# Performance work log

Hardware: AMD Instinct MI355X
Metric: run time of the kernel (lower is better)

The kernel has to match this reference:

```python
import jax, jax.numpy as jnp
import numpy as np
import math

B, T, DIM = 4, 4096, 1024
HID = int(DIM * 1.5)  # 1536
K = 4                  # conv kernel size
S = 16                 # num_slots
D = 384                # slot_dim


def setup_inputs() -> dict:
    key = jax.random.key(0)
    ks = jax.random.split(key, 16)
    inp = {
        "x": jax.random.normal(ks[0], (B, T, DIM), jnp.float32),
        "input_w": jax.random.normal(ks[1], (2 * HID, DIM), jnp.float32) * DIM ** -0.5,
        "conv_w": jax.random.normal(ks[2], (HID, K), jnp.float32) * K ** -0.5,
        "conv_b": jnp.zeros((HID,), jnp.float32),
        "gates_w": jax.random.normal(ks[3], (2 * HID, HID), jnp.float32) * HID ** -0.5,
        "gates_b": jnp.zeros((2 * HID,), jnp.float32),
        "forget_base": jnp.linspace(-4.323, -9.0, HID).astype(jnp.float32),
        "output_w": jax.random.normal(ks[4], (DIM, HID), jnp.float32) * HID ** -0.5,
        "memory_slots": jax.random.normal(ks[5], (S, D), jnp.float32) * 0.02,
        "wq_w": jax.random.normal(ks[6], (D, D), jnp.float32) * 0.02,
        "wk_w": jax.random.normal(ks[7], (D, HID), jnp.float32) * 0.02,
        "wv_w": jax.random.normal(ks[8], (D, HID), jnp.float32) * 0.02,
        "wg_w": jax.random.normal(ks[9], (1, HID), jnp.float32) * 0.02,
        "rq_w": jax.random.normal(ks[10], (D, HID), jnp.float32) * 0.02,
        "rk_w": jax.random.normal(ks[11], (D, D), jnp.float32) * 0.02,
        "rv_w": jax.random.normal(ks[12], (HID, D), jnp.float32) * 0.02,
    }
    return inp


def _causal_dwconv(x, w, b):
    # x: [B,T,H], w: [H,K], b: [H]; torch Conv1d(padding=K-1) then [:, :T] == causal
    xp = jnp.pad(x, ((0, 0), (K - 1, 0), (0, 0)))
    taps = jnp.stack([xp[:, j:j + T, :] for j in range(K)], axis=-1)  # [B,T,H,K]
    return jnp.einsum('bthk,hk->bth', taps, w) + b


def _scan(alpha, x):
    # h_t = alpha_t * h_{t-1} + x_t, elementwise over channels; along axis 1 (time)
    def combine(c1, c2):
        a1, b1 = c1
        a2, b2 = c2
        return a1 * a2, a2 * b1 + b2
    return jax.lax.associative_scan(combine, (alpha, x), axis=1)[1]


def reference(x, input_w, conv_w, conv_b, gates_w, gates_b, forget_base, output_w,
              memory_slots, wq_w, wk_w, wv_w, wg_w, rq_w, rk_w, rv_w):
    L = T // S  # segment length
    proj = x @ input_w.T                       # [B,T,2H]
    gate, xh = proj[..., :HID], proj[..., HID:]
    xh = _causal_dwconv(xh, conv_w, conv_b)    # [B,T,H]
    g = xh @ gates_w.T + gates_b               # [B,T,2H]
    forget, inp = g[..., :HID], g[..., HID:]
    alpha = jnp.exp(-8.0 * jax.nn.softplus(forget_base) * jax.nn.sigmoid(forget))
    xh = jnp.sqrt(1.0 - alpha ** 2 + 1e-6) * jax.nn.sigmoid(inp) * xh
    h = _scan(alpha, xh)                       # [B,T,H]
    xh = gate * jax.nn.sigmoid(gate) * xh      # silu-gated

    # ---- write_memory(xh) ----
    xseg = xh.reshape(B, S, L, HID)
    q = memory_slots @ wq_w.T                  # [S,D]
    kmat = jnp.einsum('bslh,dh->bsld', xseg, wk_w)
    vmat = jnp.einsum('bslh,dh->bsld', xseg, wv_w)
    qk = jnp.einsum('sd,bsld->bsl', q, kmat) / math.sqrt(D)
    attn = jax.nn.softmax(qk, axis=-1)
    mem = jnp.einsum('bsl,bsld->bsd', attn, vmat)  # [B,S,D]

    # ---- read_memory(gelu(xh)*h, mem) ----
    xr = jax.nn.gelu(xh, approximate=False) * h    # [B,T,H]
    rq = xr @ rq_w.T                               # [B,T,D]
    rk = mem @ rk_w.T                              # [B,S,D]
    rv = mem @ rv_w.T                              # [B,S,H]
    qk2 = jnp.einsum('btd,bsd->bts', rq, rk) / math.sqrt(D)
    seg = jnp.arange(T) // L
    mask = seg[:, None] <= jnp.arange(S)[None, :]  # [T,S]
    qk2 = jnp.where(mask[None], qk2, -jnp.inf)
    attn2 = jax.nn.softmax(qk2, axis=-1)
    out = jnp.einsum('bts,bsh->bth', attn2, rv)
    out = jax.nn.sigmoid(xr @ wg_w.T) * out        # write_gate on xr
    return out @ output_w.T                        # [B,T,DIM]
```

## Files before the change

### kernel.cpp

```cpp
#include <hip/hip_runtime.h>
#include <math.h>

#define BB 4
#define TT 4096
#define DIMW 1024
#define HID 1536
#define HID2 3072
#define KC 4
#define SSEG 16
#define LSEG 256
#define DD 384
#define NCH 64
#define CHL 64
#define TH  ((size_t)TT*(size_t)HID)
#define RKVN (DD + HID)

typedef _Float16 h8 __attribute__((ext_vector_type(8)));
typedef float f4 __attribute__((ext_vector_type(4)));

#define RSCL 4.8828125e-4f

__device__ __forceinline__ void hsplit(float a, _Float16& h0, _Float16& h1)
{
    _Float16 t = (_Float16)a;
    float tf = (float)t;
    if (fabsf(tf) < 6.103515625e-05f) { t = (_Float16)0.f; tf = 0.f; }
    h0 = t;
    h1 = (_Float16)((a - tf) * 2048.0f);
}

__device__ __forceinline__ void gl_lds16(const _Float16* g, _Float16* l)
{
    __builtin_amdgcn_global_load_lds(
        (const __attribute__((address_space(1))) unsigned int*)g,
        (__attribute__((address_space(3))) unsigned int*)l,
        16, 0, 0);
}

__global__ __launch_bounds__(256) void split2t(const float* __restrict__ src,
                                               _Float16* __restrict__ dst,
                                               int R, int Kd, size_t ps)
{
    __shared__ float tile[64][65];
    const int tid = threadIdx.x;
    const int bx = blockIdx.x;
    const int by = blockIdx.y;
    {
        const int lr = tid >> 2;
        const int lc = (tid & 3) * 16;
        const float* s = src + (size_t)(by * 64 + lr) * Kd + bx * 64 + lc;
#pragma unroll
        for (int e = 0; e < 16; e++) tile[lr][lc + e] = s[e];
    }
    __syncthreads();
    const int c = tid >> 5;
    const int r0 = tid & 31;
#pragma unroll
    for (int rr = 0; rr < 2; rr++) {
        const int r = r0 + rr * 32;
        h8 h0v, h1v;
#pragma unroll
        for (int e = 0; e < 8; e++) {
            _Float16 a0, a1;
            hsplit(tile[r][c * 8 + e], a0, a1);
            h0v[e] = a0; h1v[e] = a1;
        }
        const size_t didx = ((size_t)(bx * 8 + c) * R + by * 64 + r) * 8;
        *(h8*)(dst + didx) = h0v;
        *(h8*)(dst + ps + didx) = h1v;
    }
}

__global__ __launch_bounds__(256) void ccat2_kernel(const float* __restrict__ s1, int n1,
                                                    const float* __restrict__ s2, int n2,
                                                    float* __restrict__ dst)
{
    int i = blockIdx.x * 256 + threadIdx.x;
    if (i < n1) dst[i] = s1[i];
    else if (i < n1 + n2) dst[i] = s2[i - n1];
}

template<int MODE, int TM, int TN, int WRN, int WCN>
__global__ __launch_bounds__(WRN * WCN * 64, 2) void gemm_mfma(
    const _Float16* __restrict__ Ap, size_t aps,
    const _Float16* __restrict__ Wp, size_t wps,
    float* __restrict__ C0, float* __restrict__ C1,
    const float* __restrict__ X,
    _Float16* __restrict__ OP, size_t ops,
    const double* __restrict__ SPB, const float* __restrict__ GB,
    int M, int Nout, int Kd)
{
    constexpr int NWAVE = WRN * WCN;
    constexpr int WTM = TM / WRN, WTN = TN / WCN;
    constexpr int MI = WTM / 16, NI = WTN / 16;
    constexpr int API = TM / 16;
    constexpr int BPI = TN / 16;
    constexpr int ATOT = 2 * API;
    constexpr int NISS = ATOT + 2 * BPI;
    static_assert(NISS % NWAVE == 0, "issue count must divide waves");
    static_assert(MI * NI <= 16, "DUAL only");

    __shared__ _Float16 Als[2][2][TM * 32];
    __shared__ _Float16 Bls[2][2][TN * 32];

    const int tid = threadIdx.x;
    const int lane = tid & 63;
    const int wv = tid >> 6;
    const int wr = wv / WCN, wc = wv % WCN;
    const int lr = lane & 15, lg = lane >> 4;

    int bx = blockIdx.x, by = blockIdx.y;
    {
        const int gx = gridDim.x;
        const int nwg = gx * gridDim.y;
        if ((nwg & 7) == 0) {
            int wg = by * gx + bx;
            wg = (wg & 7) * (nwg >> 3) + (wg >> 3);
            bx = wg % gx; by = wg / gx;
        }
    }
    const int m0 = bx * TM, n0 = by * TN;

    f4 acc1[MI][NI], acc2[MI][NI];
#pragma unroll
    for (int i = 0; i < MI; i++)
#pragma unroll
        for (int j = 0; j < NI; j++) {
            acc1[i][j] = (f4){0.f, 0.f, 0.f, 0.f};
            acc2[i][j] = (f4){0.f, 0.f, 0.f, 0.f};
        }

    auto stage = [&](int kq0, int buf) {
#pragma unroll
        for (int j = 0; j < NISS / NWAVE; j++) {
            const int i = j * NWAVE + wv;
            if (i < ATOT) {
                const int pl = i / API, s = i - pl * API;
                const int kc = (s * 64) / TM, r0 = (s * 64) % TM;
                gl_lds16(Ap + pl * aps + ((size_t)(kq0 + kc) * M + m0 + r0) * 8 + lane * 8,
                         &Als[buf][pl][(kc * TM + r0) * 8]);
            } else {
                const int jj = i - ATOT;
                const int pl = jj / BPI, s = jj - pl * BPI;
                const int kc = (s * 64) / TN, r0 = (s * 64) % TN;
                gl_lds16(Wp + pl * wps + ((size_t)(kq0 + kc) * Nout + n0 + r0) * 8 + lane * 8,
                         &Bls[buf][pl][(kc * TN + r0) * 8]);
            }
        }
    };

    stage(0, 0);
    __syncthreads();

    const int NS = Kd / 32;
    for (int t = 0; t < NS; t++) {
        const int buf = t & 1;
        if (t + 1 < NS) stage((t + 1) * 4, buf ^ 1);

        h8 af0[MI], af1[MI];
#pragma unroll
        for (int mi = 0; mi < MI; mi++) {
            const int arow = wr * WTM + mi * 16 + lr;
            af0[mi] = *(const h8*)&Als[buf][0][(lg * TM + arow) * 8];
            af1[mi] = *(const h8*)&Als[buf][1][(lg * TM + arow) * 8];
        }
#pragma unroll
        for (int ni = 0; ni < NI; ni++) {
            const int brow = wc * WTN + ni * 16 + lr;
            h8 b0 = *(const h8*)&Bls[buf][0][(lg * TN + brow) * 8];
            h8 b1 = *(const h8*)&Bls[buf][1][(lg * TN + brow) * 8];
#pragma unroll
            for (int mi = 0; mi < MI; mi++) {
                acc1[mi][ni] = __builtin_amdgcn_mfma_f32_16x16x32_f16(af0[mi], b0, acc1[mi][ni], 0, 0, 0);
                acc2[mi][ni] = __builtin_amdgcn_mfma_f32_16x16x32_f16(af1[mi], b0, acc2[mi][ni], 0, 0, 0);
                acc2[mi][ni] = __builtin_amdgcn_mfma_f32_16x16x32_f16(af0[mi], b1, acc2[mi][ni], 0, 0, 0);
            }
        }
        __syncthreads();
    }

#pragma unroll
    for (int mi = 0; mi < MI; mi++) {
#pragma unroll
        for (int ni = 0; ni < NI; ni++) {
#pragma unroll
            for (int r = 0; r < 4; r++) {
                const float v = acc1[mi][ni][r] + acc2[mi][ni][r] * RSCL;
                const int m = m0 + wr * WTM + mi * 16 + lg * 4 + r;
                const int n = n0 + wc * WTN + ni * 16 + lr;
                if constexpr (MODE == 3) {
                    if (n < HID) {
                        double f = (double)v + (double)GB[n];
                        double sigf = 1.0 / (1.0 + exp(-f));
                        C0[(size_t)m * HID + n] = (float)exp(-8.0 * SPB[n] * sigf);
                    } else {
                        C1[(size_t)m * HID + (n - HID)] = v;
                    }
                } else if constexpr (MODE == 2) {
                    float g = v;
                    float fv = (g / (1.0f + expf(-g))) * X[(size_t)m * Nout + n];
                    C0[(size_t)m * Nout + n] = fv;
                    _Float16 a0, a1;
                    hsplit(fv, a0, a1);
                    const size_t didx = ((size_t)(n >> 3) * M + m) * 8 + (n & 7);
                    OP[didx] = a0;
                    OP[ops + didx] = a1;
                } else {
                    C0[(size_t)m * Nout + n] = v;
                }
            }
        }
    }
}

template<int TM, int TN>
__global__ __launch_bounds__(256) void gemm32(const float* __restrict__ A,
                                              const float* __restrict__ W,
                                              float* __restrict__ C0,
                                              int M, int Nout, int Kd)
{
    constexpr int GM = TM / 64;
    constexpr int GN = TN / 64;
    constexpr int AF4 = TM * 4;
    constexpr int WF4 = TN * 4;
    constexpr int ALOOP = (AF4 + 255) / 256;
    constexpr int WLOOP = (WF4 + 255) / 256;

    __shared__ float As[16][TM];
    __shared__ float Bs[16][TN];

    const int tid = threadIdx.x;
    const int m0 = blockIdx.x * TM;
    const int n0 = blockIdx.y * TN;
    const int tx = tid & 15, ty = tid >> 4;

    float acc[GM * 4][GN * 4];
#pragma unroll
    for (int i = 0; i < GM * 4; i++)
#pragma unroll
        for (int j = 0; j < GN * 4; j++) acc[i][j] = 0.0f;

    float4 aReg[ALOOP], wReg[WLOOP];

    auto issueLoads = [&](int k0) {
#pragma unroll
        for (int u = 0; u < ALOOP; u++) {
            const int idx = tid + u * 256;
            float4 v = make_float4(0.f, 0.f, 0.f, 0.f);
            if (idx < AF4) {
                const int row = idx >> 2, kq = (idx & 3) * 4;
                const long ar = (long)(m0 + row);
                if (ar < M) v = *(const float4*)(A + ar * (long)Kd + (k0 + kq));
            }
            aReg[u] = v;
        }
#pragma unroll
        for (int u = 0; u < WLOOP; u++) {
            const int idx = tid + u * 256;
            float4 v = make_float4(0.f, 0.f, 0.f, 0.f);
            if (idx < WF4) {
                const int row = idx >> 2, kq = (idx & 3) * 4;
                const long wr = (long)(n0 + row);
                if (wr < Nout) v = *(const float4*)(W + wr * (long)Kd + (k0 + kq));
            }
            wReg[u] = v;
        }
    };
    auto writeLDS = [&]() {
#pragma unroll
        for (int u = 0; u < ALOOP; u++) {
            const int idx = tid + u * 256;
            if (idx < AF4) {
                const int row = idx >> 2, kq = (idx & 3) * 4;
                As[kq + 0][row] = aReg[u].x;
                As[kq + 1][row] = aReg[u].y;
                As[kq + 2][row] = aReg[u].z;
                As[kq + 3][row] = aReg[u].w;
            }
        }
#pragma unroll
        for (int u = 0; u < WLOOP; u++) {
            const int idx = tid + u * 256;
            if (idx < WF4) {
                const int row = idx >> 2, kq = (idx & 3) * 4;
                Bs[kq + 0][row] = wReg[u].x;
                Bs[kq + 1][row] = wReg[u].y;
                Bs[kq + 2][row] = wReg[u].z;
                Bs[kq + 3][row] = wReg[u].w;
            }
        }
    };

    issueLoads(0);
    writeLDS();
    __syncthreads();

    const int NT = Kd / 16;
    for (int t = 0; t < NT; t++) {
        if (t + 1 < NT) issueLoads((t + 1) * 16);
#pragma unroll
        for (int k = 0; k < 16; k++) {
            float a[GM * 4], b[GN * 4];
#pragma unroll
            for (int g = 0; g < GM; g++) {
                const float4 t4 = *(const float4*)&As[k][g * 64 + ty * 4];
                a[g * 4 + 0] = t4.x; a[g * 4 + 1] = t4.y;
                a[g * 4 + 2] = t4.z; a[g * 4 + 3] = t4.w;
            }
#pragma unroll
            for (int g = 0; g < GN; g++) {
                const float4 t4 = *(const float4*)&Bs[k][g * 64 + tx * 4];
                b[g * 4 + 0] = t4.x; b[g * 4 + 1] = t4.y;
                b[g * 4 + 2] = t4.z; b[g * 4 + 3] = t4.w;
            }
#pragma unroll
            for (int i = 0; i < GM * 4; i++)
#pragma unroll
                for (int j = 0; j < GN * 4; j++) acc[i][j] += a[i] * b[j];
        }
        __syncthreads();
        if (t + 1 < NT) {
            writeLDS();
            __syncthreads();
        }
    }

#pragma unroll
    for (int i = 0; i < GM * 4; i++) {
        const int m = m0 + (i >> 2) * 64 + ty * 4 + (i & 3);
        if (m >= M) continue;
#pragma unroll
        for (int j = 0; j < GN * 4; j++) {
            const int n = n0 + (j >> 2) * 64 + tx * 4 + (j & 3);
            if (n >= Nout) continue;
            C0[(long)m * Nout + n] = acc[i][j];
        }
    }
}

__global__ __launch_bounds__(256) void spb_kernel(const float* __restrict__ fb,
                                                  double* __restrict__ spb)
{
    int h = blockIdx.x * 256 + threadIdx.x;
    if (h < HID) {
        double xv = (double)fb[h];
        spb[h] = log1p(exp(xv));
    }
}

__global__ __launch_bounds__(256) void conv_kernel(const float* __restrict__ xin,
                                                   const float* __restrict__ cw,
                                                   const float* __restrict__ cb,
                                                   float* __restrict__ outp,
                                                   _Float16* __restrict__ outP,
                                                   size_t ps)
{
    size_t i = (size_t)blockIdx.x * 256 + threadIdx.x;
    if (i >= TH) return;
    int h = (int)(i % HID);
    int t = (int)(i / HID);
    float acc = cb[h];
#pragma unroll
    for (int j = 0; j < KC; j++) {
        int tt = t - (KC - 1) + j;
        if (tt >= 0) acc = fmaf(cw[h * KC + j], xin[(size_t)tt * HID + h], acc);
    }
    outp[i] = acc;
    _Float16 a0, a1;
    hsplit(acc, a0, a1);
    const size_t didx = ((size_t)(h >> 3) * TT + t) * 8 + (h & 7);
    outP[didx] = a0;
    outP[ps + didx] = a1;
}

__global__ __launch_bounds__(256) void xh2_kernel(const float* __restrict__ alpha,
                                                  float* __restrict__ ip,
                                                  const float* __restrict__ xh1,
                                                  const float* __restrict__ gb)
{
    size_t i = (size_t)blockIdx.x * 256 + threadIdx.x;
    if (i >= TH) return;
    int h = (int)(i % HID);
    float a = alpha[i];
    float g2 = ip[i] + gb[HID + h];
    float s2 = sqrtf(1.0f - a * a + 1e-6f);
    float sigi = 1.0f / (1.0f + expf(-g2));
    ip[i] = s2 * sigi * xh1[i];
}

__global__ __launch_bounds__(256) void scan1_kernel(const float* __restrict__ alpha,
                                                    const float* __restrict__ xh2,
                                                    double* __restrict__ cA,
                                                    double* __restrict__ cB)
{
    int idx = blockIdx.x * 256 + threadIdx.x;
    if (idx >= NCH * HID) return;
    int h = idx % HID;
    int c = idx / HID;
    size_t base = (size_t)c * CHL * HID + h;
    double aP = 1.0, bV = 0.0;
    for (int i = 0; i < CHL; i++) {
        double a  = (double)alpha[base + (size_t)i * HID];
        double xv = (double)xh2 [base + (size_t)i * HID];
        bV = a * bV + xv;
        aP *= a;
    }
    size_t o = (size_t)c * HID + h;
    cA[o] = aP;
    cB[o] = bV;
}

__global__ __launch_bounds__(256) void scan2_kernel(const double* __restrict__ cA,
                                                    const double* __restrict__ cB,
                                                    double* __restrict__ cH0)
{
    int h = blockIdx.x * 256 + threadIdx.x;
    if (h >= HID) return;
    double carry = 0.0;
    for (int c = 0; c < NCH; c++) {
        size_t o = (size_t)c * HID + h;
        cH0[o] = carry;
        carry = cA[o] * carry + cB[o];
    }
}

__global__ __launch_bounds__(256) void scan3_kernel(const float* __restrict__ alpha,
                                                    const float* __restrict__ xh2,
                                                    const double* __restrict__ cH0,
                                                    float* __restrict__ hout)
{
    int idx = blockIdx.x * 256 + threadIdx.x;
    if (idx >= NCH * HID) return;
    int h = idx % HID;
    int c = idx / HID;
    size_t base = (size_t)c * CHL * HID + h;
    double hv = cH0[(size_t)c * HID + h];
    for (int i = 0; i < CHL; i++) {
        double a  = (double)alpha[base + (size_t)i * HID];
        double xv = (double)xh2 [base + (size_t)i * HID];
        hv = a * hv + xv;
        hout[base + (size_t)i * HID] = (float)hv;
    }
}

__global__ __launch_bounds__(256) void gelu_mul_kernel(float* __restrict__ xh3,
                                                       const float* __restrict__ hbuf,
                                                       _Float16* __restrict__ outP,
                                                       size_t ps)
{
    size_t i = (size_t)blockIdx.x * 256 + threadIdx.x;
    if (i >= TH) return;
    int h = (int)(i % HID);
    int t = (int)(i / HID);
    float x3 = xh3[i];
    float ge = 0.5f * x3 * (1.0f + erff(x3 * 0.70710678f));
    float fv = ge * hbuf[i];
    xh3[i] = fv;
    _Float16 a0, a1;
    hsplit(fv, a0, a1);
    const size_t didx = ((size_t)(h >> 3) * TT + t) * 8 + (h & 7);
    outP[didx] = a0;
    outP[ps + didx] = a1;
}

__global__ __launch_bounds__(256) void attn1_kernel(const float* __restrict__ kv,
                                                    const float* __restrict__ qbuf,
                                                    float* __restrict__ mem)
{
    const int s = blockIdx.x;
    const int l = threadIdx.x;
    const size_t row = (size_t)s * LSEG + l;
    const float* kr = kv + row * (2 * DD);
    const float* qs = qbuf + (size_t)s * DD;
    double acc = 0.0;
    for (int d = 0; d < DD; d++) acc += (double)qs[d] * (double)kr[d];
    double qk = acc / sqrt((double)DD);
    __shared__ double r1[256];
    __shared__ double sw[256];
    r1[l] = qk; __syncthreads();
    for (int off = 128; off > 0; off >>= 1) {
        if (l < off) r1[l] = fmax(r1[l], r1[l + off]);
        __syncthreads();
    }
    double m = r1[0]; __syncthreads();
    double e = exp(qk - m);
    r1[l] = e; __syncthreads();
    for (int off = 128; off > 0; off >>= 1) {
        if (l < off) r1[l] += r1[l + off];
        __syncthreads();
    }
    double denom = r1[0];
    sw[l] = e / denom; __syncthreads();
    const size_t vbase = (size_t)s * LSEG * (2 * DD) + DD;
    for (int d = l; d < DD; d += 256) {
        double a2 = 0.0;
        for (int ll = 0; ll < LSEG; ll++)
            a2 += sw[ll] * (double)kv[vbase + (size_t)ll * (2 * DD) + d];
        mem[(size_t)s * DD + d] = (float)a2;
    }
}

__global__ __launch_bounds__(256) void attn2_kernel(const float* __restrict__ rq,
                                                    const float* __restrict__ rkv,
                                                    const float* __restrict__ xr,
                                                    const float* __restrict__ wg,
                                                    _Float16* __restrict__ outP,
                                                    size_t ps)
{
    const int t = blockIdx.x;
    const int sigma = t >> 8;
    const int tid = threadIdx.x;
    __shared__ double sqk[16];
    __shared__ double red[256];
    __shared__ double sw[16];
    __shared__ double sgate;

    const float* rqn = rq + (size_t)t * DD;
    {
        int s = tid >> 4, j = tid & 15;
        const float* rks = rkv + (size_t)s * RKVN;
        double part = 0.0;
        for (int d = j; d < DD; d += 16) part += (double)rqn[d] * (double)rks[d];
#pragma unroll
        for (int off = 8; off > 0; off >>= 1) part += __shfl_down(part, off, 16);
        if (j == 0) sqk[s] = part;
    }
    double gp = 0.0;
    const float* xrn = xr + (size_t)t * HID;
    for (int hh = tid; hh < HID; hh += 256) gp += (double)xrn[hh] * (double)wg[hh];
    red[tid] = gp; __syncthreads();
    for (int off = 128; off > 0; off >>= 1) {
        if (tid < off) red[tid] += red[tid + off];
        __syncthreads();
    }
    if (tid == 0) {
        const double inv = 1.0 / sqrt((double)DD);
        double m = -1e300;
        for (int ss = sigma; ss < 16; ss++) {
            double v = sqk[ss] * inv;
            sqk[ss] = v;
            if (v > m) m = v;
        }
        double sum = 0.0;
        for (int ss = sigma; ss < 16; ss++) {
            double e = exp(sqk[ss] - m);
            sw[ss] = e;
            sum += e;
        }
        double isum = 1.0 / sum;
        for (int ss = 0; ss < sigma; ss++) sw[ss] = 0.0;
        for (int ss = sigma; ss < 16; ss++) sw[ss] *= isum;
        sgate = 1.0 / (1.0 + exp(-red[0]));
    }
    __syncthreads();
    const double gte = sgate;
    for (int c = tid; c < HID / 8; c += 256) {
        double accv[8] = {0, 0, 0, 0, 0, 0, 0, 0};
        for (int ss = sigma; ss < 16; ss++) {
            const float* rvp = rkv + (size_t)ss * RKVN + DD + c * 8;
            double w = sw[ss];
#pragma unroll
            for (int e = 0; e < 8; e++) accv[e] += w * (double)rvp[e];
        }
        h8 h0v, h1v;
#pragma unroll
        for (int e = 0; e < 8; e++) {
            _Float16 a0, a1;
            hsplit((float)(gte * accv[e]), a0, a1);
            h0v[e] = a0; h1v[e] = a1;
        }
        const size_t didx = ((size_t)c * TT + t) * 8;
        *(h8*)(outP + didx) = h0v;
        *(h8*)(outP + ps + didx) = h1v;
    }
}

extern "C" void kernel_launch(void* const* d_in, const int* in_sizes, int n_in,
                              void* d_out, int out_size, void* d_ws, size_t ws_size,
                              hipStream_t stream)
{
    const float* x            = (const float*)d_in[0];
    const float* input_w      = (const float*)d_in[1];
    const float* conv_w       = (const float*)d_in[2];
    const float* conv_b       = (const float*)d_in[3];
    const float* gates_w      = (const float*)d_in[4];
    const float* gates_b      = (const float*)d_in[5];
    const float* forget_base  = (const float*)d_in[6];
    const float* output_w     = (const float*)d_in[7];
    const float* memory_slots = (const float*)d_in[8];
    const float* wq_w         = (const float*)d_in[9];
    const float* wk_w         = (const float*)d_in[10];
    const float* wv_w         = (const float*)d_in[11];
    const float* wg_w         = (const float*)d_in[12];
    const float* rq_w         = (const float*)d_in[13];
    const float* rk_w         = (const float*)d_in[14];
    const float* rv_w         = (const float*)d_in[15];
    float* out = (float*)d_out;

    double* spb  = (double*)d_ws;
    double* cA   = spb + HID;
    double* cB   = cA + (size_t)NCH * HID;
    double* cH0  = cB + (size_t)NCH * HID;
    float* slotA = (float*)(cH0 + (size_t)NCH * HID);
    float* slotB = slotA + TH;
    float* slotC = slotB + TH;
    float* qbuf   = slotC + TH;
    float* membuf = qbuf + (size_t)SSEG * DD;
    float* rkvw   = membuf + (size_t)SSEG * DD;
    float* rkvbuf = rkvw + (size_t)RKVN * DD;

    _Float16* base_h = (_Float16*)(rkvbuf + (size_t)SSEG * RKVN);
    const size_t iwN  = (size_t)HID * DIMW;
    const size_t gwN  = (size_t)HID2 * HID;
    const size_t kvN  = (size_t)(2 * DD) * HID;
    const size_t rqN  = (size_t)DD * HID;
    const size_t owN  = (size_t)DIMW * HID;
    const size_t xbN  = (size_t)TT * DIMW;
    _Float16* iwlo = base_h;
    _Float16* iwhi = iwlo + 2 * iwN;
    _Float16* gwp  = iwhi + 2 * iwN;
    _Float16* wkvp = gwp  + 2 * gwN;
    _Float16* rqwp = wkvp + 2 * kvN;
    _Float16* owp  = rqwp + 2 * rqN;
    _Float16* xbP  = owp  + 2 * owN;
    _Float16* P1   = xbP  + 2 * xbN;

    dim3 blk(256);
    const int ewBlocks = (int)(TH / 256);

    spb_kernel<<<(HID + 255) / 256, blk, 0, stream>>>(forget_base, spb);
    ccat2_kernel<<<(2 * DD * HID + 255) / 256, blk, 0, stream>>>(
        wk_w, DD * HID, wv_w, DD * HID, slotA);
    ccat2_kernel<<<(RKVN * DD + 255) / 256, blk, 0, stream>>>(
        rk_w, DD * DD, rv_w, HID * DD, rkvw);
    split2t<<<dim3(DIMW / 64, HID / 64), blk, 0, stream>>>(input_w, iwlo, HID, DIMW, iwN);
    split2t<<<dim3(DIMW / 64, HID / 64), blk, 0, stream>>>(input_w + (size_t)HID * DIMW,
                                                           iwhi, HID, DIMW, iwN);
    split2t<<<dim3(HID / 64, HID2 / 64), blk, 0, stream>>>(gates_w, gwp, HID2, HID, gwN);
    split2t<<<dim3(HID / 64, (2 * DD) / 64), blk, 0, stream>>>(slotA, wkvp, 2 * DD, HID, kvN);
    split2t<<<dim3(HID / 64, DD / 64), blk, 0, stream>>>(rq_w, rqwp, DD, HID, rqN);
    split2t<<<dim3(HID / 64, DIMW / 64), blk, 0, stream>>>(output_w, owp, DIMW, HID, owN);
    gemm32<64, 64><<<dim3(1, DD / 64), blk, 0, stream>>>(
        memory_slots, wq_w, qbuf, SSEG, DD, DD);

    for (int b = 0; b < BB; b++) {
        const float* xb   = x   + (size_t)b * TT * DIMW;
        float*       outb = out + (size_t)b * TT * DIMW;

        split2t<<<dim3(DIMW / 64, TT / 64), blk, 0, stream>>>(xb, xbP, TT, DIMW, xbN);
        gemm_mfma<0, 128, 128, 2, 2><<<dim3(TT / 128, HID / 128), blk, 0, stream>>>(
            xbP, xbN, iwhi, iwN, slotB, (float*)nullptr, (const float*)nullptr,
            (_Float16*)nullptr, 0, (const double*)nullptr, (const float*)nullptr,
            TT, HID, DIMW);
        conv_kernel<<<ewBlocks, blk, 0, stream>>>(slotB, conv_w, conv_b, slotC, P1, TH);
        gemm_mfma<3, 128, 128, 2, 2><<<dim3(TT / 128, HID2 / 128), blk, 0, stream>>>(
            P1, TH, gwp, gwN, slotA, slotB, (const float*)nullptr,
            (_Float16*)nullptr, 0, spb, gates_b, TT, HID2, HID);
        xh2_kernel<<<ewBlocks, blk, 0, stream>>>(slotA, slotB, slotC, gates_b);
        scan1_kernel<<<(NCH * HID) / 256, blk, 0, stream>>>(slotA, slotB, cA, cB);
        scan2_kernel<<<(HID + 255) / 256, blk, 0, stream>>>(cA, cB, cH0);
        scan3_kernel<<<(NCH * HID) / 256, blk, 0, stream>>>(slotA, slotB, cH0, slotC);
        gemm_mfma<2, 128, 128, 2, 2><<<dim3(TT / 128, HID / 128), blk, 0, stream>>>(
            xbP, xbN, iwlo, iwN, slotA, (float*)nullptr, slotB, P1, TH,
            (const double*)nullptr, (const float*)nullptr, TT, HID, DIMW);
        gemm_mfma<0, 128, 128, 2, 2><<<dim3(TT / 128, (2 * DD) / 128), blk, 0, stream>>>(
            P1, TH, wkvp, kvN, slotB, (float*)nullptr, (const float*)nullptr,
            (_Float16*)nullptr, 0, (const double*)nullptr, (const float*)nullptr,
            TT, 2 * DD, HID);
        attn1_kernel<<<SSEG, blk, 0, stream>>>(slotB, qbuf, membuf);
        gelu_mul_kernel<<<ewBlocks, blk, 0, stream>>>(slotA, slotC, P1, TH);
        gemm_mfma<0, 64, 128, 2, 2><<<dim3(TT / 64, DD / 128), blk, 0, stream>>>(
            P1, TH, rqwp, rqN, slotB, (float*)nullptr, (const float*)nullptr,
            (_Float16*)nullptr, 0, (const double*)nullptr, (const float*)nullptr,
            TT, DD, HID);
        gemm32<64, 64><<<dim3(1, (RKVN + 63) / 64), blk, 0, stream>>>(
            membuf, rkvw, rkvbuf, SSEG, RKVN, DD);
        attn2_kernel<<<TT, blk, 0, stream>>>(slotB, rkvbuf, slotA, wg_w, P1, TH);
        gemm_mfma<0, 128, 128, 2, 2><<<dim3(TT / 128, DIMW / 128), blk, 0, stream>>>(
            P1, TH, owp, owN, outb, (float*)nullptr, (const float*)nullptr,
            (_Float16*)nullptr, 0, (const double*)nullptr, (const float*)nullptr,
            TT, DIMW, HID);
    }
}
```

Before: 2.659 ms.

## Use 8-wave GEMM blocks, move alpha epilogue out, fuse scan3 with gelu

```diff
diff --git a/kernel.cpp b/kernel.cpp
--- a/kernel.cpp
+++ b/kernel.cpp
@@ -80,25 +80,24 @@
     else if (i < n1 + n2) dst[i] = s2[i - n1];
 }
 
-template<int MODE, int TM, int TN, int WRN, int WCN>
-__global__ __launch_bounds__(WRN * WCN * 64, 2) void gemm_mfma(
+template<int MODE, int TM, int TN>
+__global__ __launch_bounds__(512, 4) void gemm_mfma(
     const _Float16* __restrict__ Ap, size_t aps,
     const _Float16* __restrict__ Wp, size_t wps,
     float* __restrict__ C0, float* __restrict__ C1,
     const float* __restrict__ X,
     _Float16* __restrict__ OP, size_t ops,
-    const double* __restrict__ SPB, const float* __restrict__ GB,
     int M, int Nout, int Kd)
 {
-    constexpr int NWAVE = WRN * WCN;
-    constexpr int WTM = TM / WRN, WTN = TN / WCN;
+    constexpr int WTM = TM / 2, WTN = TN / 4;
     constexpr int MI = WTM / 16, NI = WTN / 16;
+    static_assert(MI * NI <= 16, "DUAL only");
     constexpr int API = TM / 16;
     constexpr int BPI = TN / 16;
     constexpr int ATOT = 2 * API;
     constexpr int NISS = ATOT + 2 * BPI;
-    static_assert(NISS % NWAVE == 0, "issue count must divide waves");
-    static_assert(MI * NI <= 16, "DUAL only");
+    static_assert(NISS % 8 == 0, "issue count must divide 8 waves");
+    constexpr int PW = NISS / 8;
 
     __shared__ _Float16 Als[2][2][TM * 32];
     __shared__ _Float16 Bls[2][2][TN * 32];
@@ -106,7 +105,7 @@
     const int tid = threadIdx.x;
     const int lane = tid & 63;
     const int wv = tid >> 6;
-    const int wr = wv / WCN, wc = wv % WCN;
+    const int wr = wv >> 2, wc = wv & 3;
     const int lr = lane & 15, lg = lane >> 4;
 
     int bx = blockIdx.x, by = blockIdx.y;
@@ -132,8 +131,8 @@
 
     auto stage = [&](int kq0, int buf) {
 #pragma unroll
-        for (int j = 0; j < NISS / NWAVE; j++) {
-            const int i = j * NWAVE + wv;
+        for (int j = 0; j < PW; j++) {
+            const int i = j * 8 + wv;
             if (i < ATOT) {
                 const int pl = i / API, s = i - pl * API;
                 const int kc = (s * 64) / TM, r0 = (s * 64) % TM;
@@ -188,14 +187,9 @@
                 const float v = acc1[mi][ni][r] + acc2[mi][ni][r] * RSCL;
                 const int m = m0 + wr * WTM + mi * 16 + lg * 4 + r;
                 const int n = n0 + wc * WTN + ni * 16 + lr;
-                if constexpr (MODE == 3) {
-                    if (n < HID) {
-                        double f = (double)v + (double)GB[n];
-                        double sigf = 1.0 / (1.0 + exp(-f));
-                        C0[(size_t)m * HID + n] = (float)exp(-8.0 * SPB[n] * sigf);
-                    } else {
-                        C1[(size_t)m * HID + (n - HID)] = v;
-                    }
+                if constexpr (MODE == 1) {
+                    if (n < HID) C0[(size_t)m * HID + n] = v;
+                    else         C1[(size_t)m * HID + (n - HID)] = v;
                 } else if constexpr (MODE == 2) {
                     float g = v;
                     float fv = (g / (1.0f + expf(-g))) * X[(size_t)m * Nout + n];
@@ -373,18 +367,22 @@
     outP[ps + didx] = a1;
 }
 
-__global__ __launch_bounds__(256) void xh2_kernel(const float* __restrict__ alpha,
-                                                  float* __restrict__ ip,
-                                                  const float* __restrict__ xh1,
-                                                  const float* __restrict__ gb)
+__global__ __launch_bounds__(256) void alpha_xh2_kernel(float* __restrict__ fg,
+                                                        float* __restrict__ ip,
+                                                        const float* __restrict__ xh1,
+                                                        const double* __restrict__ spb,
+                                                        const float* __restrict__ gb)
 {
     size_t i = (size_t)blockIdx.x * 256 + threadIdx.x;
     if (i >= TH) return;
     int h = (int)(i % HID);
-    float a = alpha[i];
+    double f  = (double)fg[i] + (double)gb[h];
     float g2 = ip[i] + gb[HID + h];
-    float s2 = sqrtf(1.0f - a * a + 1e-6f);
+    double sigf = 1.0 / (1.0 + exp(-f));
+    float alpha = (float)exp(-8.0 * spb[h] * sigf);
+    float s2 = sqrtf(1.0f - alpha * alpha + 1e-6f);
     float sigi = 1.0f / (1.0f + expf(-g2));
+    fg[i] = alpha;
     ip[i] = s2 * sigi * xh1[i];
 }
 
@@ -424,10 +422,12 @@
     }
 }
 
-__global__ __launch_bounds__(256) void scan3_kernel(const float* __restrict__ alpha,
-                                                    const float* __restrict__ xh2,
-                                                    const double* __restrict__ cH0,
-                                                    float* __restrict__ hout)
+__global__ __launch_bounds__(256) void scan3gelu_kernel(const float* __restrict__ alpha,
+                                                        const float* __restrict__ xh2,
+                                                        const double* __restrict__ cH0,
+                                                        float* __restrict__ xh3,
+                                                        _Float16* __restrict__ outP,
+                                                        size_t ps)
 {
     int idx = blockIdx.x * 256 + threadIdx.x;
     if (idx >= NCH * HID) return;
@@ -436,31 +436,21 @@
     size_t base = (size_t)c * CHL * HID + h;
     double hv = cH0[(size_t)c * HID + h];
     for (int i = 0; i < CHL; i++) {
-        double a  = (double)alpha[base + (size_t)i * HID];
-        double xv = (double)xh2 [base + (size_t)i * HID];
+        size_t off = base + (size_t)i * HID;
+        double a  = (double)alpha[off];
+        double xv = (double)xh2 [off];
         hv = a * hv + xv;
-        hout[base + (size_t)i * HID] = (float)hv;
-    }
-}
-
-__global__ __launch_bounds__(256) void gelu_mul_kernel(float* __restrict__ xh3,
-                                                       const float* __restrict__ hbuf,
-                                                       _Float16* __restrict__ outP,
-                                                       size_t ps)
-{
-    size_t i = (size_t)blockIdx.x * 256 + threadIdx.x;
-    if (i >= TH) return;
-    int h = (int)(i % HID);
-    int t = (int)(i / HID);
-    float x3 = xh3[i];
-    float ge = 0.5f * x3 * (1.0f + erff(x3 * 0.70710678f));
-    float fv = ge * hbuf[i];
-    xh3[i] = fv;
-    _Float16 a0, a1;
-    hsplit(fv, a0, a1);
-    const size_t didx = ((size_t)(h >> 3) * TT + t) * 8 + (h & 7);
-    outP[didx] = a0;
-    outP[ps + didx] = a1;
+        float x3 = xh3[off];
+        float ge = 0.5f * x3 * (1.0f + erff(x3 * 0.70710678f));
+        float fv = ge * (float)hv;
+        xh3[off] = fv;
+        _Float16 a0, a1;
+        hsplit(fv, a0, a1);
+        const int t = c * CHL + i;
+        const size_t didx = ((size_t)(h >> 3) * TT + t) * 8 + (h & 7);
+        outP[didx] = a0;
+        outP[ps + didx] = a1;
+    }
 }
 
 __global__ __launch_bounds__(256) void attn1_kernel(const float* __restrict__ kv,
@@ -608,8 +598,9 @@
     float* membuf = qbuf + (size_t)SSEG * DD;
     float* rkvw   = membuf + (size_t)SSEG * DD;
     float* rkvbuf = rkvw + (size_t)RKVN * DD;
-
-    _Float16* base_h = (_Float16*)(rkvbuf + (size_t)SSEG * RKVN);
+    float* kvbuf  = rkvbuf + (size_t)SSEG * RKVN;
+
+    _Float16* base_h = (_Float16*)(kvbuf + (size_t)TT * 2 * DD);
     const size_t iwN  = (size_t)HID * DIMW;
     const size_t gwN  = (size_t)HID2 * HID;
     const size_t kvN  = (size_t)(2 * DD) * HID;
@@ -626,6 +617,7 @@
     _Float16* P1   = xbP  + 2 * xbN;
 
     dim3 blk(256);
+    dim3 blk512(512);
     const int ewBlocks = (int)(TH / 256);
 
     spb_kernel<<<(HID + 255) / 256, blk, 0, stream>>>(forget_base, spb);
@@ -648,37 +640,32 @@
         float*       outb = out + (size_t)b * TT * DIMW;
 
         split2t<<<dim3(DIMW / 64, TT / 64), blk, 0, stream>>>(xb, xbP, TT, DIMW, xbN);
-        gemm_mfma<0, 128, 128, 2, 2><<<dim3(TT / 128, HID / 128), blk, 0, stream>>>(
+        gemm_mfma<0, 128, 128><<<dim3(TT / 128, HID / 128), blk512, 0, stream>>>(
             xbP, xbN, iwhi, iwN, slotB, (float*)nullptr, (const float*)nullptr,
-            (_Float16*)nullptr, 0, (const double*)nullptr, (const float*)nullptr,
-            TT, HID, DIMW);
+            (_Float16*)nullptr, 0, TT, HID, DIMW);
         conv_kernel<<<ewBlocks, blk, 0, stream>>>(slotB, conv_w, conv_b, slotC, P1, TH);
-        gemm_mfma<3, 128, 128, 2, 2><<<dim3(TT / 128, HID2 / 128), blk, 0, stream>>>(
+        gemm_mfma<1, 128, 128><<<dim3(TT / 128, HID2 / 128), blk512, 0, stream>>>(
             P1, TH, gwp, gwN, slotA, slotB, (const float*)nullptr,
-            (_Float16*)nullptr, 0, spb, gates_b, TT, HID2, HID);
-        xh2_kernel<<<ewBlocks, blk, 0, stream>>>(slotA, slotB, slotC, gates_b);
+            (_Float16*)nullptr, 0, TT, HID2, HID);
+        alpha_xh2_kernel<<<ewBlocks, blk, 0, stream>>>(slotA, slotB, slotC, spb, gates_b);
         scan1_kernel<<<(NCH * HID) / 256, blk, 0, stream>>>(slotA, slotB, cA, cB);
         scan2_kernel<<<(HID + 255) / 256, blk, 0, stream>>>(cA, cB, cH0);
-        scan3_kernel<<<(NCH * HID) / 256, blk, 0, stream>>>(slotA, slotB, cH0, slotC);
-        gemm_mfma<2, 128, 128, 2, 2><<<dim3(TT / 128, HID / 128), blk, 0, stream>>>(
-            xbP, xbN, iwlo, iwN, slotA, (float*)nullptr, slotB, P1, TH,
-            (const double*)nullptr, (const float*)nullptr, TT, HID, DIMW);
-        gemm_mfma<0, 128, 128, 2, 2><<<dim3(TT / 128, (2 * DD) / 128), blk, 0, stream>>>(
-            P1, TH, wkvp, kvN, slotB, (float*)nullptr, (const float*)nullptr,
-            (_Float16*)nullptr, 0, (const double*)nullptr, (const float*)nullptr,
-            TT, 2 * DD, HID);
-        attn1_kernel<<<SSEG, blk, 0, stream>>>(slotB, qbuf, membuf);
-        gelu_mul_kernel<<<ewBlocks, blk, 0, stream>>>(slotA, slotC, P1, TH);
-        gemm_mfma<0, 64, 128, 2, 2><<<dim3(TT / 64, DD / 128), blk, 0, stream>>>(
-            P1, TH, rqwp, rqN, slotB, (float*)nullptr, (const float*)nullptr,
-            (_Float16*)nullptr, 0, (const double*)nullptr, (const float*)nullptr,
-            TT, DD, HID);
+        gemm_mfma<2, 128, 128><<<dim3(TT / 128, HID / 128), blk512, 0, stream>>>(
+            xbP, xbN, iwlo, iwN, slotC, (float*)nullptr, slotB, P1, TH, TT, HID, DIMW);
+        gemm_mfma<0, 128, 128><<<dim3(TT / 128, (2 * DD) / 128), blk512, 0, stream>>>(
+            P1, TH, wkvp, kvN, kvbuf, (float*)nullptr, (const float*)nullptr,
+            (_Float16*)nullptr, 0, TT, 2 * DD, HID);
+        attn1_kernel<<<SSEG, blk, 0, stream>>>(kvbuf, qbuf, membuf);
         gemm32<64, 64><<<dim3(1, (RKVN + 63) / 64), blk, 0, stream>>>(
             membuf, rkvw, rkvbuf, SSEG, RKVN, DD);
-        attn2_kernel<<<TT, blk, 0, stream>>>(slotB, rkvbuf, slotA, wg_w, P1, TH);
-        gemm_mfma<0, 128, 128, 2, 2><<<dim3(TT / 128, DIMW / 128), blk, 0, stream>>>(
+        scan3gelu_kernel<<<(NCH * HID) / 256, blk, 0, stream>>>(
+            slotA, slotB, cH0, slotC, P1, TH);
+        gemm_mfma<0, 64, 128><<<dim3(TT / 64, DD / 128), blk512, 0, stream>>>(
+            P1, TH, rqwp, rqN, slotB, (float*)nullptr, (const float*)nullptr,
+            (_Float16*)nullptr, 0, TT, DD, HID);
+        attn2_kernel<<<TT, blk, 0, stream>>>(slotB, rkvbuf, slotC, wg_w, P1, TH);
+        gemm_mfma<0, 128, 128><<<dim3(TT / 128, DIMW / 128), blk512, 0, stream>>>(
             P1, TH, owp, owN, outb, (float*)nullptr, (const float*)nullptr,
-            (_Float16*)nullptr, 0, (const double*)nullptr, (const float*)nullptr,
-            TT, DIMW, HID);
-    }
-}
+            (_Float16*)nullptr, 0, TT, DIMW, HID);
+    }
+}
```

Result: faster. 2.474 ms (-7.0%).
